# Performance work log

Measured on AMD Instinct MI355X. Metric: run time of the kernel, lower is better.

The kernel has to match this reference:

```python
import jax, jax.numpy as jnp
import numpy as np

N_LIST = [2048, 2048]
N_CUM = np.cumsum([0] + N_LIST)


def _chamfer(xo, yo):
    # xo: [B, M, 3], yo: [B, N, 3]
    diff = xo[:, :, None, :] - yo[:, None, :, :]        # [B, M, N, 3]
    dist = jnp.sqrt(jnp.sum(diff * diff, axis=-1))       # [B, M, N]
    mean_x = jnp.mean(jnp.min(dist, axis=2))             # x -> nearest y
    mean_y = jnp.mean(jnp.min(dist, axis=1))             # y -> nearest x
    return mean_x + mean_y


def setup_inputs() -> dict:
    key = jax.random.key(0)
    kx, ky = jax.random.split(key)
    x = jax.random.normal(kx, (8, 4096, 3), dtype=jnp.float32)
    y = jax.random.normal(ky, (8, 4096, 3), dtype=jnp.float32)
    return {"x": x, "y": y}


def reference(x, y):
    # loss_type='chamfer', probability=1 -> top-k over ALL distances == plain mean.
    loss = jnp.float32(0.0)
    for i in range(len(N_LIST)):
        lo, hi = int(N_CUM[i]), int(N_CUM[i + 1])
        loss = loss + _chamfer(x[:, lo:hi], y[:, lo:hi])
    return loss
```

## Files before the change

### kernel.cpp

```cpp
#include <hip/hip_runtime.h>
#include <math.h>

typedef float v2f __attribute__((ext_vector_type(2)));

#if __has_builtin(__builtin_elementwise_fma)
#define FMA2(a, b, c) __builtin_elementwise_fma((a), (b), (c))
#else
static __device__ __forceinline__ v2f FMA2(v2f a, v2f b, v2f c) {
    v2f r; r.x = fmaf(a.x, b.x, c.x); r.y = fmaf(a.y, b.y, c.y); return r;
}
#endif

#define NBATCH 8
#define PTOT   4096
#define NG     2048
#define S      16
#define SLEN   (NG / S)
#define QPT    8
#define NT     256
#define NPROB  32
#define NBLK1  (NPROB * S)
#define NPART  (NPROB * S * NG)

__global__ __launch_bounds__(256) void chamfer_pass1(
    const float* __restrict__ x, const float* __restrict__ y,
    float* __restrict__ pmin)
{
    __shared__ float  raw[SLEN * 3];
    __shared__ float4 refX[SLEN / 4];
    __shared__ float4 refY[SLEN / 4];
    __shared__ float4 refZ[SLEN / 4];
    __shared__ float4 refW[SLEN / 4];

    const int blk   = blockIdx.x;
    const int tid   = threadIdx.x;
    const int slice = blk & (S - 1);
    const int prob  = blk >> 4;
    const int dir   = prob >> 4;
    const int bg    = prob & 15;
    const int b     = bg >> 1;
    const int g     = bg & 1;

    const float* qb = (dir == 0 ? x : y) + (size_t)(b * PTOT + g * NG) * 3;
    const float* rb = (dir == 0 ? y : x) + (size_t)(b * PTOT + g * NG) * 3;

    if (tid < (SLEN * 3) / 4) {
        float4 v = ((const float4*)(rb + slice * SLEN * 3))[tid];
        ((float4*)raw)[tid] = v;
    }

    float4 qv[6];
    {
        const float4* qp = (const float4*)(qb + (size_t)tid * QPT * 3);
        #pragma unroll
        for (int i = 0; i < 6; i++) qv[i] = qp[i];
    }

    __syncthreads();

    if (tid < SLEN / 4) {
        const float* p = raw + tid * 12;
        float x0 = p[0], y0 = p[1],  z0 = p[2];
        float x1 = p[3], y1 = p[4],  z1 = p[5];
        float x2 = p[6], y2 = p[7],  z2 = p[8];
        float x3 = p[9], y3 = p[10], z3 = p[11];
        refX[tid] = make_float4(x0, x1, x2, x3);
        refY[tid] = make_float4(y0, y1, y2, y3);
        refZ[tid] = make_float4(z0, z1, z2, z3);
        refW[tid] = make_float4(fmaf(x0, x0, fmaf(y0, y0, z0 * z0)),
                                fmaf(x1, x1, fmaf(y1, y1, z1 * z1)),
                                fmaf(x2, x2, fmaf(y2, y2, z2 * z2)),
                                fmaf(x3, x3, fmaf(y3, y3, z3 * z3)));
    }

    v2f ax2[QPT], ay2[QPT], az2[QPT];
    float qn[QPT], mn[QPT];
    const float* qf = reinterpret_cast<const float*>(qv);
    #pragma unroll
    for (int k = 0; k < QPT; k++) {
        float qx = qf[k * 3 + 0];
        float qy = qf[k * 3 + 1];
        float qz = qf[k * 3 + 2];
        float ax = -2.0f * qx, ay = -2.0f * qy, az = -2.0f * qz;
        ax2[k] = (v2f){ax, ax};
        ay2[k] = (v2f){ay, ay};
        az2[k] = (v2f){az, az};
        qn[k] = fmaf(qx, qx, fmaf(qy, qy, qz * qz));
        mn[k] = 3.4e38f;
    }

    __syncthreads();

    #pragma unroll 2
    for (int n4 = 0; n4 < SLEN / 4; n4++) {
        float4 X = refX[n4], Y = refY[n4], Z = refZ[n4], W = refW[n4];
        v2f X01 = (v2f){X.x, X.y}, X23 = (v2f){X.z, X.w};
        v2f Y01 = (v2f){Y.x, Y.y}, Y23 = (v2f){Y.z, Y.w};
        v2f Z01 = (v2f){Z.x, Z.y}, Z23 = (v2f){Z.z, Z.w};
        v2f W01 = (v2f){W.x, W.y}, W23 = (v2f){W.z, W.w};
        #pragma unroll
        for (int k = 0; k < QPT; k++) {
            v2f t01 = FMA2(X01, ax2[k], W01);
            t01     = FMA2(Y01, ay2[k], t01);
            t01     = FMA2(Z01, az2[k], t01);
            v2f t23 = FMA2(X23, ax2[k], W23);
            t23     = FMA2(Y23, ay2[k], t23);
            t23     = FMA2(Z23, az2[k], t23);
            mn[k] = fminf(fminf(t01.x, t01.y), mn[k]);
            mn[k] = fminf(fminf(t23.x, t23.y), mn[k]);
        }
    }

    float* op = pmin + (size_t)(prob * S + slice) * NG + tid * QPT;
    #pragma unroll
    for (int k = 0; k < QPT; k++)
        op[k] = mn[k] + qn[k];
}

__global__ __launch_bounds__(256) void chamfer_pass2(
    const float* __restrict__ pmin, float* __restrict__ bsum)
{
    __shared__ float s4[4];
    const int gid  = blockIdx.x * 256 + threadIdx.x;
    const int prob = gid >> 11;
    const int q    = gid & (NG - 1);

    float m0 = 3.4e38f, m1 = 3.4e38f;
    #pragma unroll
    for (int s = 0; s < S; s += 2) {
        m0 = fminf(m0, pmin[(size_t)(prob * S + s) * NG + q]);
        m1 = fminf(m1, pmin[(size_t)(prob * S + s + 1) * NG + q]);
    }
    float m = fminf(m0, m1);

    float d = sqrtf(fmaxf(m, 0.0f));

    for (int off = 32; off > 0; off >>= 1)
        d += __shfl_down(d, off, 64);
    if ((threadIdx.x & 63) == 0) s4[threadIdx.x >> 6] = d;
    __syncthreads();
    if (threadIdx.x == 0)
        bsum[blockIdx.x] = (s4[0] + s4[1]) + (s4[2] + s4[3]);
}

__global__ __launch_bounds__(256) void chamfer_pass3(
    const float* __restrict__ bsum, float* __restrict__ out)
{
    __shared__ float s4[4];
    const int tid = threadIdx.x;
    float v = bsum[tid];
    for (int off = 32; off > 0; off >>= 1)
        v += __shfl_down(v, off, 64);
    if ((tid & 63) == 0) s4[tid >> 6] = v;
    __syncthreads();
    if (tid == 0)
        out[0] = ((s4[0] + s4[1]) + (s4[2] + s4[3])) * (1.0f / 16384.0f);
}

extern "C" void kernel_launch(void* const* d_in, const int* in_sizes, int n_in,
                              void* d_out, int out_size, void* d_ws, size_t ws_size,
                              hipStream_t stream) {
    const float* x = (const float*)d_in[0];
    const float* y = (const float*)d_in[1];
    float* out  = (float*)d_out;
    float* pmin = (float*)d_ws;
    float* bsum = pmin + NPART;

    chamfer_pass1<<<NBLK1, NT, 0, stream>>>(x, y, pmin);
    chamfer_pass2<<<256, NT, 0, stream>>>(pmin, bsum);
    chamfer_pass3<<<1, NT, 0, stream>>>(bsum, out);
}
```

Measured before the change: 21.83 us.

## Double reference slices, use inline packed FMA asm, recompute norms in loop

Doubles the number of reference slices so pass1 launches twice as many blocks, each handling half as many reference points, and sets an occupancy hint of 4 blocks per CU. Replaces the FMA builtin with inline v_pk_fma_f32/v_pk_mul_f32 asm and computes reference squared norms inside the inner loop instead of storing them in shared memory. Also vectorizes the partial-min stores to float4 and widens the pass2 min loop. The cost is twice the partial-min workspace traffic read by pass2, plus a few extra ALU ops per reference group.

```diff
diff --git a/kernel.cpp b/kernel.cpp
--- a/kernel.cpp
+++ b/kernel.cpp
@@ -3,18 +3,21 @@
 
 typedef float v2f __attribute__((ext_vector_type(2)));
 
-#if __has_builtin(__builtin_elementwise_fma)
-#define FMA2(a, b, c) __builtin_elementwise_fma((a), (b), (c))
-#else
-static __device__ __forceinline__ v2f FMA2(v2f a, v2f b, v2f c) {
-    v2f r; r.x = fmaf(a.x, b.x, c.x); r.y = fmaf(a.y, b.y, c.y); return r;
+static __device__ __forceinline__ v2f pkfma(v2f a, v2f b, v2f c) {
+    v2f d;
+    asm("v_pk_fma_f32 %0, %1, %2, %3" : "=v"(d) : "v"(a), "v"(b), "v"(c));
+    return d;
 }
-#endif
+static __device__ __forceinline__ v2f pkmul(v2f a, v2f b) {
+    v2f d;
+    asm("v_pk_mul_f32 %0, %1, %2" : "=v"(d) : "v"(a), "v"(b));
+    return d;
+}
 
 #define NBATCH 8
 #define PTOT   4096
 #define NG     2048
-#define S      16
+#define S      32
 #define SLEN   (NG / S)
 #define QPT    8
 #define NT     256
@@ -22,7 +25,7 @@
 #define NBLK1  (NPROB * S)
 #define NPART  (NPROB * S * NG)
 
-__global__ __launch_bounds__(256) void chamfer_pass1(
+__global__ __launch_bounds__(256, 4) void chamfer_pass1(
     const float* __restrict__ x, const float* __restrict__ y,
     float* __restrict__ pmin)
 {
@@ -30,12 +33,11 @@
     __shared__ float4 refX[SLEN / 4];
     __shared__ float4 refY[SLEN / 4];
     __shared__ float4 refZ[SLEN / 4];
-    __shared__ float4 refW[SLEN / 4];
 
     const int blk   = blockIdx.x;
     const int tid   = threadIdx.x;
     const int slice = blk & (S - 1);
-    const int prob  = blk >> 4;
+    const int prob  = blk >> 5;
     const int dir   = prob >> 4;
     const int bg    = prob & 15;
     const int b     = bg >> 1;
@@ -44,7 +46,7 @@
     const float* qb = (dir == 0 ? x : y) + (size_t)(b * PTOT + g * NG) * 3;
     const float* rb = (dir == 0 ? y : x) + (size_t)(b * PTOT + g * NG) * 3;
 
-    if (tid < (SLEN * 3) / 4) {
+    if (tid < 48) {
         float4 v = ((const float4*)(rb + slice * SLEN * 3))[tid];
         ((float4*)raw)[tid] = v;
     }
@@ -60,17 +62,9 @@
 
     if (tid < SLEN / 4) {
         const float* p = raw + tid * 12;
-        float x0 = p[0], y0 = p[1],  z0 = p[2];
-        float x1 = p[3], y1 = p[4],  z1 = p[5];
-        float x2 = p[6], y2 = p[7],  z2 = p[8];
-        float x3 = p[9], y3 = p[10], z3 = p[11];
-        refX[tid] = make_float4(x0, x1, x2, x3);
-        refY[tid] = make_float4(y0, y1, y2, y3);
-        refZ[tid] = make_float4(z0, z1, z2, z3);
-        refW[tid] = make_float4(fmaf(x0, x0, fmaf(y0, y0, z0 * z0)),
-                                fmaf(x1, x1, fmaf(y1, y1, z1 * z1)),
-                                fmaf(x2, x2, fmaf(y2, y2, z2 * z2)),
-                                fmaf(x3, x3, fmaf(y3, y3, z3 * z3)));
+        refX[tid] = make_float4(p[0], p[3], p[6], p[9]);
+        refY[tid] = make_float4(p[1], p[4], p[7], p[10]);
+        refZ[tid] = make_float4(p[2], p[5], p[8], p[11]);
     }
 
     v2f ax2[QPT], ay2[QPT], az2[QPT];
@@ -93,19 +87,24 @@
 
     #pragma unroll 2
     for (int n4 = 0; n4 < SLEN / 4; n4++) {
-        float4 X = refX[n4], Y = refY[n4], Z = refZ[n4], W = refW[n4];
+        float4 X = refX[n4], Y = refY[n4], Z = refZ[n4];
         v2f X01 = (v2f){X.x, X.y}, X23 = (v2f){X.z, X.w};
         v2f Y01 = (v2f){Y.x, Y.y}, Y23 = (v2f){Y.z, Y.w};
         v2f Z01 = (v2f){Z.x, Z.y}, Z23 = (v2f){Z.z, Z.w};
-        v2f W01 = (v2f){W.x, W.y}, W23 = (v2f){W.z, W.w};
+        v2f W01 = pkmul(X01, X01);
+        W01 = pkfma(Y01, Y01, W01);
+        W01 = pkfma(Z01, Z01, W01);
+        v2f W23 = pkmul(X23, X23);
+        W23 = pkfma(Y23, Y23, W23);
+        W23 = pkfma(Z23, Z23, W23);
         #pragma unroll
         for (int k = 0; k < QPT; k++) {
-            v2f t01 = FMA2(X01, ax2[k], W01);
-            t01     = FMA2(Y01, ay2[k], t01);
-            t01     = FMA2(Z01, az2[k], t01);
-            v2f t23 = FMA2(X23, ax2[k], W23);
-            t23     = FMA2(Y23, ay2[k], t23);
-            t23     = FMA2(Z23, az2[k], t23);
+            v2f t01 = pkfma(X01, ax2[k], W01);
+            t01     = pkfma(Y01, ay2[k], t01);
+            t01     = pkfma(Z01, az2[k], t01);
+            v2f t23 = pkfma(X23, ax2[k], W23);
+            t23     = pkfma(Y23, ay2[k], t23);
+            t23     = pkfma(Z23, az2[k], t23);
             mn[k] = fminf(fminf(t01.x, t01.y), mn[k]);
             mn[k] = fminf(fminf(t23.x, t23.y), mn[k]);
         }
@@ -113,8 +112,11 @@
 
     float* op = pmin + (size_t)(prob * S + slice) * NG + tid * QPT;
     #pragma unroll
-    for (int k = 0; k < QPT; k++)
-        op[k] = mn[k] + qn[k];
+    for (int i = 0; i < 2; i++)
+        ((float4*)op)[i] = make_float4(mn[4*i+0] + qn[4*i+0],
+                                       mn[4*i+1] + qn[4*i+1],
+                                       mn[4*i+2] + qn[4*i+2],
+                                       mn[4*i+3] + qn[4*i+3]);
 }
 
 __global__ __launch_bounds__(256) void chamfer_pass2(
@@ -127,9 +129,13 @@
 
     float m0 = 3.4e38f, m1 = 3.4e38f;
     #pragma unroll
-    for (int s = 0; s < S; s += 2) {
-        m0 = fminf(m0, pmin[(size_t)(prob * S + s) * NG + q]);
-        m1 = fminf(m1, pmin[(size_t)(prob * S + s + 1) * NG + q]);
+    for (int s = 0; s < S; s += 4) {
+        float l0 = pmin[(size_t)(prob * S + s + 0) * NG + q];
+        float l1 = pmin[(size_t)(prob * S + s + 1) * NG + q];
+        float l2 = pmin[(size_t)(prob * S + s + 2) * NG + q];
+        float l3 = pmin[(size_t)(prob * S + s + 3) * NG + q];
+        m0 = fminf(fminf(l0, l1), m0);
+        m1 = fminf(fminf(l2, l3), m1);
     }
     float m = fminf(m0, m1);
 
```

New measurement: 24.46 us. 1.12x slower.
